# Performance work log

Hardware: AMD Instinct MI355X
Metric: run time of the kernel (lower is better)

The kernel has to match this reference:

```python
import jax, jax.numpy as jnp
import numpy as np
from jax import lax

H = 64      # hidden_size
VOC = 512   # num_embedding
L = 2       # num_layers


def layernorm(x, g, b, eps=1e-5):
    mu = jnp.mean(x, axis=-1, keepdims=True)
    var = jnp.mean((x - mu) ** 2, axis=-1, keepdims=True)
    return (x - mu) * lax.rsqrt(var + eps) * g + b


def conv3d(x, w, b):
    # x: [B, U, V, W, Cin] (channels-last), w: [3,3,3,Cin,Cout]
    return lax.conv_general_dilated(
        x, w, (1, 1, 1), 'SAME',
        dimension_numbers=('NDHWC', 'DHWIO', 'NDHWC')) + b


def setup_inputs() -> dict:
    key = jax.random.key(0)
    ks = jax.random.split(key, 8)
    f = lambda k, s, sc: jax.random.normal(k, s, jnp.float32) * sc
    return {
        'code': jax.random.randint(ks[0], (2, 5, 1, 8, 8, 8), 0, VOC),
        'ncode': jax.random.randint(ks[1], (2, 3, 1, 8, 8, 8), 0, VOC),
        'emb': f(ks[2], (VOC, H), 0.02),
        'win': f(ks[3], (L, 3, 3, 3, H, 4 * H), 0.05),
        'bin_': jnp.zeros((L, 4 * H), jnp.float32),
        'gin_w': jnp.ones((L, 4 * H), jnp.float32),
        'gin_b': jnp.zeros((L, 4 * H), jnp.float32),
        'wh': f(ks[4], (L, 3, 3, 3, H, 4 * H), 0.05),
        'bh': jnp.zeros((L, 4 * H), jnp.float32),
        'gh_w': jnp.ones((L, 4 * H), jnp.float32),
        'gh_b': jnp.zeros((L, 4 * H), jnp.float32),
        'w1': f(ks[5], (H, H), 0.05),
        'b1': jnp.zeros((H,), jnp.float32),
        'ln_g': jnp.ones((H,), jnp.float32),
        'ln_b': jnp.zeros((H,), jnp.float32),
        'w2': f(ks[6], (H, VOC), 0.05),
        'b2': jnp.zeros((VOC,), jnp.float32),
    }


def _forward(code, ncode, emb, win, bin_, gin_w, gin_b, wh, bh, gh_w, gh_b,
             w1, b1, ln_g, ln_b, w2, b2):
    N, Sn, C, U, V, W = ncode.shape
    x = jnp.concatenate([code, ncode[:, :-1]], axis=1)  # [N,S,C,U,V,W]
    S = x.shape[1]
    x = jnp.transpose(x, (0, 2, 1, 3, 4, 5)).reshape(N * C, S, U, V, W)
    h = emb[x]  # [NC, S, U, V, W, H]
    Hd = h.shape[-1]
    for i in range(L):
        # input-path conv is recurrence-free: batch it over all timesteps
        gi = layernorm(conv3d(h.reshape(N * C * S, U, V, W, Hd), win[i], bin_[i]),
                       gin_w[i], gin_b[i])
        gi = jnp.moveaxis(gi.reshape(N * C, S, U, V, W, 4 * Hd), 1, 0)  # [S,NC,U,V,W,4H]

        def step(carry, g, i=i):
            hx, cx = carry
            gates = g + layernorm(conv3d(hx, wh[i], bh[i]), gh_w[i], gh_b[i])
            ig, fg, cg, og = jnp.split(gates, 4, axis=-1)
            cx = jax.nn.sigmoid(fg) * cx + jax.nn.sigmoid(ig) * jnp.tanh(cg)
            hx = jax.nn.sigmoid(og) * jnp.tanh(cx)
            return (hx, cx), hx

        z = jnp.zeros((N * C, U, V, W, Hd), h.dtype)
        _, ys = lax.scan(step, (z, z), gi)
        h = jnp.moveaxis(ys, 0, 1)  # [NC,S,U,V,W,H]
    h = h[:, -Sn:].reshape(N, C, Sn, U, V, W, Hd)
    h = jnp.transpose(h, (0, 2, 1, 3, 4, 5, 6))  # [N,Sn,C,U,V,W,H]
    z = jax.nn.gelu(layernorm(h @ w1 + b1, ln_g, ln_b), approximate=False)
    logits = z @ w2 + b2  # [N,Sn,C,U,V,W,VOC]
    score = jnp.transpose(logits, (0, 6, 1, 2, 3, 4, 5))  # [N,VOC,Sn,C,U,V,W]
    logp = jax.nn.log_softmax(logits, axis=-1)
    loss = -jnp.mean(jnp.take_along_axis(logp, ncode[..., None], axis=-1))
    pred = jnp.argmax(score, axis=1)
    return score, loss, pred


def reference(code, ncode, emb, win, bin_, gin_w, gin_b, wh, bh, gh_w, gh_b,
              w1, b1, ln_g, ln_b, w2, b2):
    return _forward(code, ncode, emb, win, bin_, gin_w, gin_b, wh, bh,
                    gh_w, gh_b, w1, b1, ln_g, ln_b, w2, b2)
```

## Files before the change

### kernel.cpp

```cpp
#include <hip/hip_runtime.h>


typedef _Float16 f16;
typedef _Float16 f16x8 __attribute__((ext_vector_type(8)));
typedef float    f32x4 __attribute__((ext_vector_type(4)));

#define WSTRIDE 442368
#define WPT     884736
#define XSP     65536
#define HSP     458752
#define GPART   262144

__device__ __forceinline__ float wred_sum(float v) {
    #pragma unroll
    for (int o = 32; o > 0; o >>= 1) v += __shfl_down(v, o, 64);
    return __shfl(v, 0, 64);
}
__device__ __forceinline__ float fsig(float x)  { return 1.f / (1.f + __expf(-x)); }
__device__ __forceinline__ float ftanh(float x) { return 1.f - 2.f / (__expf(2.f*x) + 1.f); }

__global__ __launch_bounds__(256) void embed_kernel(
    const int* __restrict__ code, const int* __restrict__ ncode,
    const float* __restrict__ emb, f16* __restrict__ h)
{
    int e = blockIdx.x * 256 + threadIdx.x;
    int ch = e & 63;
    int pos = e >> 6;
    int vox = pos & 511;
    int t = pos >> 9;
    int s = t % 7, nc = t / 7;
    int tok = (s < 5) ? code[(nc*5 + s)*512 + vox]
                      : ncode[(nc*3 + (s-5))*512 + vox];
    float x = emb[tok*64 + ch];
    f16 hi = (f16)x;
    h[(size_t)pos*128 + ch]      = hi;
    h[(size_t)pos*128 + 64 + ch] = (f16)(x - (float)hi);
}

__global__ __launch_bounds__(256) void wsplit_kernel(
    const float* __restrict__ win, const float* __restrict__ wh,
    f16* __restrict__ wp)
{
    int b = blockIdx.x;
    int tensor = b / 27, tap = b % 27;
    const float* src = ((tensor & 1) ? wh : win) + (tensor >> 1) * WSTRIDE
                     + tap * 16384;
    int co = threadIdx.x;
    int sw = co & 7;
    #pragma unroll
    for (int hs = 0; hs < 2; ++hs) {
        f16* dst = wp + (((size_t)tensor*27 + tap)*2 + hs)*16384 + co*64;
        #pragma unroll
        for (int j = 0; j < 4; ++j) {
            f16x8 hi8, lo8;
            #pragma unroll
            for (int m = 0; m < 8; ++m) {
                float w = src[(hs*32 + j*8 + m)*256 + co] * 64.f;
                f16 hv = (f16)w;
                hi8[m] = hv;
                lo8[m] = (f16)(w - (float)hv);
            }
            *(f16x8*)(dst + ((j     ^ sw))*8) = hi8;
            *(f16x8*)(dst + (((4+j) ^ sw))*8) = lo8;
        }
    }
}

struct MJob { const f16* x; const f16* w; float* y; };
struct MJobs { MJob j[4]; };

__global__ __launch_bounds__(256, 2) void conv_mfma_kernel(MJobs js)
{
    const MJob J = js.j[blockIdx.y];
    __shared__ float4 smem[4096];
    f16* wbuf = (f16*)smem;

    const int bx = blockIdx.x;
    const int cog = bx & 3, u = (bx >> 2) & 7, slab = (bx >> 5) & 1, kb = bx >> 6;
    const int t = threadIdx.x, wid = t >> 6, l = t & 63;
    const int lv = (l >> 3) & 1, lw = l & 7, khi = l >> 4;

    const int gid = kb*4 + wid;
    const int g0  = (gid < 6) ? gid*7 : 42 + (gid - 6)*6;
    const int cnt = (gid < 6) ? 7 : 6;

    const f16* xbase = J.x + (size_t)slab * HSP;
    const f16* wjob  = J.w + (size_t)cog * 4096;
    f16* wmine = wbuf + wid * 8192;

    f16x8 wreg[8];
    auto wload = [&](int k) {
        const f16* src = wjob + (size_t)k * 16384 + l * 8;
        #pragma unroll
        for (int i = 0; i < 8; ++i) wreg[i] = *(const f16x8*)(src + i * 512);
    };
    auto wstore = [&](int b) {
        f16* dst = wmine + b * 4096 + l * 8;
        #pragma unroll
        for (int i = 0; i < 8; ++i) *(f16x8*)(dst + i * 512) = wreg[i];
    };

    wload(g0); wstore(0);

    f32x4 acc[4][4] = {};
    int cur = 0;
    for (int q = 0; q < cnt; ++q) {
        const int k = g0 + q;
        if (q + 1 < cnt) wload(k + 1);
        const int tap = k >> 1, hs = k & 1;
        const int du = tap / 9, rr = tap % 9, dv = rr / 3, dw = rr % 3;
        const int uu = u + du - 1;
        const bool uok = (unsigned)uu < 8u;
        const f16* xrow[4]; bool ok[4];
        #pragma unroll
        for (int a = 0; a < 4; ++a) {
            int vs = a*2 + lv + dv - 1, ws = lw + dw - 1;
            ok[a] = uok && (unsigned)vs < 8u && (unsigned)ws < 8u;
            xrow[a] = xbase + ((size_t)(uu*64 + vs*8 + ws) << 7) + khi*8;
        }
        const f16* wrow = wmine + cur*4096 + (l & 15)*64;
        const int schi = ((khi    ) ^ lw) * 8;
        const int sclo = ((4 + khi) ^ lw) * 8;
        f16x8 ahi[4], alo[4], bhi[4], blo[4];
        #pragma unroll
        for (int a = 0; a < 4; ++a) {
            f16x8 v = {0,0,0,0,0,0,0,0}, v2 = v;
            if (ok[a]) {
                v  = *(const f16x8*)(xrow[a] + hs*32);
                v2 = *(const f16x8*)(xrow[a] + 64 + hs*32);
            }
            ahi[a] = v; alo[a] = v2;
        }
        #pragma unroll
        for (int n = 0; n < 4; ++n) {
            bhi[n] = *(const f16x8*)(wrow + n*1024 + schi);
            blo[n] = *(const f16x8*)(wrow + n*1024 + sclo);
        }
        #pragma unroll
        for (int a = 0; a < 4; ++a)
            #pragma unroll
            for (int n = 0; n < 4; ++n)
                acc[a][n] = __builtin_amdgcn_mfma_f32_16x16x32_f16(
                    ahi[a], bhi[n], acc[a][n], 0, 0, 0);
        #pragma unroll
        for (int a = 0; a < 4; ++a)
            #pragma unroll
            for (int n = 0; n < 4; ++n)
                acc[a][n] = __builtin_amdgcn_mfma_f32_16x16x32_f16(
                    alo[a], bhi[n], acc[a][n], 0, 0, 0);
        #pragma unroll
        for (int a = 0; a < 4; ++a)
            #pragma unroll
            for (int n = 0; n < 4; ++n)
                acc[a][n] = __builtin_amdgcn_mfma_f32_16x16x32_f16(
                    ahi[a], blo[n], acc[a][n], 0, 0, 0);
        if (q + 1 < cnt) { wstore(cur ^ 1); cur ^= 1; }
    }

    f32x4* red = (f32x4*)smem;
    {
        f32x4* mine = red + (size_t)(wid * 64 + l) * 16;
        #pragma unroll
        for (int a = 0; a < 4; ++a)
            #pragma unroll
            for (int n = 0; n < 4; ++n)
                mine[(a * 4 + n) ^ (l & 15)] = acc[a][n];
    }
    __syncthreads();
    {
        float* yp = J.y + (size_t)kb * GPART;
        const int a = t >> 6, ll = t & 63;
        #pragma unroll
        for (int n = 0; n < 4; ++n) {
            const int ch = (a * 4 + n) ^ (ll & 15);
            f32x4 sv = red[(0 * 64 + ll) * 16 + ch]
                     + red[(1 * 64 + ll) * 16 + ch]
                     + red[(2 * 64 + ll) * 16 + ch]
                     + red[(3 * 64 + ll) * 16 + ch];
            const int co = cog * 64 + n * 16 + (ll & 15);
            #pragma unroll
            for (int r = 0; r < 4; ++r) {
                int vox = a * 16 + (ll >> 4) * 4 + r;
                yp[(size_t)(slab * 512 + u * 64 + vox) * 256 + co]
                    = sv[r] * 0.015625f;
            }
        }
    }
}

struct GJob {
    const float* giA; const float* giB;
    const float* ghA; const float* ghB;
    const float* bin; const float* bhb;
    const float* ginw; const float* ginb;
    const float* ghw;  const float* ghb;
    float* cx; f16* h16; int k; int k0;
};
__global__ __launch_bounds__(256) void gates_step_kernel(GJob ja, GJob jb)
{
    const GJob J = (blockIdx.y == 0) ? ja : jb;
    const int wid = threadIdx.x >> 6, lane = threadIdx.x & 63;
    const int row = blockIdx.x * 4 + wid;
    const int nc = row >> 9, vox = row & 511;

    const float* gA = J.giA + (size_t)row*256;
    const float* gB = J.giB + (size_t)row*256;
    float a0 = gA[lane]     + gB[lane]     + J.bin[lane];
    float a1 = gA[64+lane]  + gB[64+lane]  + J.bin[64+lane];
    float a2 = gA[128+lane] + gB[128+lane] + J.bin[128+lane];
    float a3 = gA[192+lane] + gB[192+lane] + J.bin[192+lane];
    float mu1 = wred_sum(a0+a1+a2+a3) * (1.f/256.f);
    float d0=a0-mu1, d1=a1-mu1, d2=a2-mu1, d3=a3-mu1;
    float v1 = wred_sum(d0*d0+d1*d1+d2*d2+d3*d3) * (1.f/256.f);
    float rs1 = rsqrtf(v1 + 1e-5f);

    float b0, b1, b2, b3;
    if (J.k0) {
        b0 = J.bhb[lane]; b1 = J.bhb[64+lane];
        b2 = J.bhb[128+lane]; b3 = J.bhb[192+lane];
    } else {
        const float* hA = J.ghA + (size_t)row*256;
        const float* hB = J.ghB + (size_t)row*256;
        b0 = hA[lane]     + hB[lane]     + J.bhb[lane];
        b1 = hA[64+lane]  + hB[64+lane]  + J.bhb[64+lane];
        b2 = hA[128+lane] + hB[128+lane] + J.bhb[128+lane];
        b3 = hA[192+lane] + hB[192+lane] + J.bhb[192+lane];
    }
    float mu2 = wred_sum(b0+b1+b2+b3) * (1.f/256.f);
    float e0=b0-mu2, e1=b1-mu2, e2=b2-mu2, e3=b3-mu2;
    float v2 = wred_sum(e0*e0+e1*e1+e2*e2+e3*e3) * (1.f/256.f);
    float rs2 = rsqrtf(v2 + 1e-5f);

    float Ig = d0*rs1*J.ginw[lane]     + J.ginb[lane]     + e0*rs2*J.ghw[lane]     + J.ghb[lane];
    float Fg = d1*rs1*J.ginw[64+lane]  + J.ginb[64+lane]  + e1*rs2*J.ghw[64+lane]  + J.ghb[64+lane];
    float Cg = d2*rs1*J.ginw[128+lane] + J.ginb[128+lane] + e2*rs2*J.ghw[128+lane] + J.ghb[128+lane];
    float Og = d3*rs1*J.ginw[192+lane] + J.ginb[192+lane] + e3*rs2*J.ghw[192+lane] + J.ghb[192+lane];

    float c_old = J.k0 ? 0.f : J.cx[(size_t)row*64 + lane];
    float c_new = fsig(Fg)*c_old + fsig(Ig)*ftanh(Cg);
    float h_new = fsig(Og)*ftanh(c_new);
    J.cx[(size_t)row*64 + lane] = c_new;
    size_t hb = ((size_t)(nc*7 + J.k)*512 + vox)*128 + lane;
    f16 hi = (f16)h_new;
    J.h16[hb]      = hi;
    J.h16[hb + 64] = (f16)(h_new - (float)hi);
}

__global__ __launch_bounds__(256) void head_kernel(
    const f16* __restrict__ h,
    const float* __restrict__ w1, const float* __restrict__ b1,
    const float* __restrict__ lng, const float* __restrict__ lnb,
    const float* __restrict__ w2, const float* __restrict__ b2,
    const int* __restrict__ ncode,
    float* __restrict__ out)
{
    __shared__ float hsm[16][64];
    __shared__ float zv[16][64];
    __shared__ float lg[10240];
    const int blk = blockIdx.x;
    const int n = blk / 96;
    const int sn = (blk / 32) % 3;
    const int vox0 = (blk & 31) * 16;
    const int t = threadIdx.x, wid = t >> 6, lane = t & 63;

    for (int idx = t; idx < 1024; idx += 256) {
        int vr = idx >> 6, ch = idx & 63;
        const f16* hv = h + (size_t)((n*7 + sn + 4)*512 + vox0 + vr)*128;
        hsm[vr][ch] = (float)hv[ch] + (float)hv[64 + ch];
    }
    __syncthreads();

    float yva[4], yvb[4];
    #pragma unroll
    for (int r = 0; r < 4; ++r) { yva[r] = b1[lane]; yvb[r] = 0.f; }
    for (int kk = 0; kk < 64; kk += 2) {
        float w1a = w1[kk*64 + lane], w1b = w1[(kk+1)*64 + lane];
        #pragma unroll
        for (int r = 0; r < 4; ++r) {
            yva[r] = fmaf(hsm[wid*4 + r][kk],     w1a, yva[r]);
            yvb[r] = fmaf(hsm[wid*4 + r][kk + 1], w1b, yvb[r]);
        }
    }
    #pragma unroll
    for (int r = 0; r < 4; ++r) {
        float yv = yva[r] + yvb[r];
        float mu = wred_sum(yv) * (1.f/64.f);
        float d = yv - mu;
        float var = wred_sum(d*d) * (1.f/64.f);
        float ln = d * rsqrtf(var + 1e-5f) * lng[lane] + lnb[lane];
        zv[wid*4 + r][lane] = 0.5f * ln * (1.f + erff(ln * 0.70710678118654752f));
    }
    __syncthreads();

    float l[4][8];
    #pragma unroll
    for (int r = 0; r < 4; ++r)
        #pragma unroll
        for (int j = 0; j < 8; ++j) l[r][j] = b2[j*64 + lane];
    for (int kk = 0; kk < 64; ++kk) {
        float wv[8];
        #pragma unroll
        for (int j = 0; j < 8; ++j) wv[j] = w2[kk*512 + j*64 + lane];
        #pragma unroll
        for (int r = 0; r < 4; ++r) {
            float zz = zv[wid*4 + r][kk];
            #pragma unroll
            for (int j = 0; j < 8; ++j) l[r][j] = fmaf(zz, wv[j], l[r][j]);
        }
    }
    #pragma unroll
    for (int r = 0; r < 4; ++r)
        #pragma unroll
        for (int j = 0; j < 8; ++j)
            lg[(j*64 + lane)*20 + wid*4 + r] = l[r][j];

    #pragma unroll
    for (int r = 0; r < 4; ++r) {
        float m = l[r][0]; int mi = lane;
        #pragma unroll
        for (int j = 1; j < 8; ++j)
            if (l[r][j] > m) { m = l[r][j]; mi = j*64 + lane; }
        #pragma unroll
        for (int o = 32; o > 0; o >>= 1) {
            float om = __shfl_down(m, o, 64);
            int   oi = __shfl_down(mi, o, 64);
            if (om > m || (om == m && oi < mi)) { m = om; mi = oi; }
        }
        float maxv = __shfl(m, 0, 64);
        int   maxi = __shfl(mi, 0, 64);
        float es = 0.f;
        #pragma unroll
        for (int j = 0; j < 8; ++j) es += __expf(l[r][j] - maxv);
        float sum = wred_sum(es);
        if (lane == 0) {
            int vox = vox0 + wid*4 + r;
            int target = ncode[(n*3 + sn)*512 + vox];
            float logp = lg[target*20 + wid*4 + r] - maxv - __logf(sum);
            atomicAdd(out + 1572864, -logp * (1.f/3072.f));
            out[1572865 + (n*3 + sn)*512 + vox] = (float)maxi;
        }
    }

    __syncthreads();
    for (int e = t; e < 2048; e += 256) {
        int co = e >> 2, p = e & 3;
        int base = co*20 + p*4;
        float4 o4 = { lg[base], lg[base+1], lg[base+2], lg[base+3] };
        *(float4*)(out + (size_t)((n*512 + co)*3 + sn)*512 + vox0 + p*4) = o4;
    }
}

extern "C" void kernel_launch(void* const* d_in, const int* in_sizes, int n_in,
                              void* d_out, int out_size, void* d_ws, size_t ws_size,
                              hipStream_t stream) {
    (void)in_sizes; (void)n_in; (void)out_size; (void)ws_size;
    const int*   code  = (const int*)d_in[0];
    const int*   ncode = (const int*)d_in[1];
    const float* emb   = (const float*)d_in[2];
    const float* win   = (const float*)d_in[3];
    const float* bin_  = (const float*)d_in[4];
    const float* gin_w = (const float*)d_in[5];
    const float* gin_b = (const float*)d_in[6];
    const float* wh    = (const float*)d_in[7];
    const float* bh    = (const float*)d_in[8];
    const float* gh_w  = (const float*)d_in[9];
    const float* gh_b  = (const float*)d_in[10];
    const float* w1    = (const float*)d_in[11];
    const float* b1    = (const float*)d_in[12];
    const float* ln_g  = (const float*)d_in[13];
    const float* ln_b  = (const float*)d_in[14];
    const float* w2    = (const float*)d_in[15];
    const float* b2    = (const float*)d_in[16];
    float* out = (float*)d_out;

    float* base  = (float*)d_ws;
    f16*   wp    = (f16*)base;
    f16*   h1    = (f16*)(base + 1769472);
    f16*   h2    = h1 + 917504;
    float* gi1   = base + 2686976;
    float* gi2   = gi1 + 2*GPART;
    float* ghat1 = gi2 + 2*GPART;
    float* ghat2 = ghat1 + 2*GPART;
    float* cx1   = ghat2 + 2*GPART;
    float* cx2   = cx1 + 65536;

    const f16* win0 = wp;
    const f16* wh0  = wp + WPT;
    const f16* win1 = wp + 2*WPT;
    const f16* wh1  = wp + 3*WPT;

    hipMemsetAsync(out + 1572864, 0, sizeof(float), stream);
    embed_kernel<<<1792, 256, 0, stream>>>(code, ncode, emb, h1);
    wsplit_kernel<<<108, 256, 0, stream>>>(win, wh, wp);

    {
        MJobs js{};
        js.j[0] = { h1, win0, gi1 };
        conv_mfma_kernel<<<dim3(128, 1), 256, 0, stream>>>(js);
    }

    for (int s = 0; s <= 7; ++s) {
        GJob g1 = { gi1, gi1 + GPART, ghat1, ghat1 + GPART, bin_, bh,
                    gin_w, gin_b, gh_w, gh_b, cx1, h1, s, s == 0 };
        GJob g2 = { gi2, gi2 + GPART, ghat2, ghat2 + GPART, bin_ + 256, bh + 256,
                    gin_w + 256, gin_b + 256, gh_w + 256, gh_b + 256,
                    cx2, h2, s - 1, s == 1 };
        if (s == 0)
            gates_step_kernel<<<dim3(256, 1), 256, 0, stream>>>(g1, g1);
        else if (s <= 6)
            gates_step_kernel<<<dim3(256, 2), 256, 0, stream>>>(g1, g2);
        else
            gates_step_kernel<<<dim3(256, 1), 256, 0, stream>>>(g2, g2);

        MJobs js{}; int nj = 0;
        if (s <= 5) js.j[nj++] = { h1 + (size_t)(s+1)*XSP, win0, gi1 };
        if (s <= 5) js.j[nj++] = { h1 + (size_t)s*XSP,     wh0,  ghat1 };
        if (s <= 6) js.j[nj++] = { h1 + (size_t)s*XSP,     win1, gi2 };
        if (s >= 1 && s <= 6)
                    js.j[nj++] = { h2 + (size_t)(s-1)*XSP, wh1,  ghat2 };
        if (nj > 0)
            conv_mfma_kernel<<<dim3(128, nj), 256, 0, stream>>>(js);
    }

    head_kernel<<<192, 256, 0, stream>>>(h2, w1, b1, ln_g, ln_b, w2, b2, ncode, out);
}
```

Before: 336.0 us.

## Split conv blocks over voxel halves, merge prep kernels, block-reduce loss atomics

```diff
diff --git a/kernel.cpp b/kernel.cpp
--- a/kernel.cpp
+++ b/kernel.cpp
@@ -19,49 +19,48 @@
 __device__ __forceinline__ float fsig(float x)  { return 1.f / (1.f + __expf(-x)); }
 __device__ __forceinline__ float ftanh(float x) { return 1.f - 2.f / (__expf(2.f*x) + 1.f); }
 
-__global__ __launch_bounds__(256) void embed_kernel(
+__global__ __launch_bounds__(256) void prep_kernel(
     const int* __restrict__ code, const int* __restrict__ ncode,
-    const float* __restrict__ emb, f16* __restrict__ h)
-{
-    int e = blockIdx.x * 256 + threadIdx.x;
-    int ch = e & 63;
-    int pos = e >> 6;
-    int vox = pos & 511;
-    int t = pos >> 9;
-    int s = t % 7, nc = t / 7;
-    int tok = (s < 5) ? code[(nc*5 + s)*512 + vox]
-                      : ncode[(nc*3 + (s-5))*512 + vox];
-    float x = emb[tok*64 + ch];
-    f16 hi = (f16)x;
-    h[(size_t)pos*128 + ch]      = hi;
-    h[(size_t)pos*128 + 64 + ch] = (f16)(x - (float)hi);
-}
-
-__global__ __launch_bounds__(256) void wsplit_kernel(
+    const float* __restrict__ emb, f16* __restrict__ h,
     const float* __restrict__ win, const float* __restrict__ wh,
     f16* __restrict__ wp)
 {
-    int b = blockIdx.x;
-    int tensor = b / 27, tap = b % 27;
-    const float* src = ((tensor & 1) ? wh : win) + (tensor >> 1) * WSTRIDE
-                     + tap * 16384;
-    int co = threadIdx.x;
-    int sw = co & 7;
-    #pragma unroll
-    for (int hs = 0; hs < 2; ++hs) {
-        f16* dst = wp + (((size_t)tensor*27 + tap)*2 + hs)*16384 + co*64;
-        #pragma unroll
-        for (int j = 0; j < 4; ++j) {
-            f16x8 hi8, lo8;
-            #pragma unroll
-            for (int m = 0; m < 8; ++m) {
-                float w = src[(hs*32 + j*8 + m)*256 + co] * 64.f;
-                f16 hv = (f16)w;
-                hi8[m] = hv;
-                lo8[m] = (f16)(w - (float)hv);
+    if (blockIdx.x < 1792) {
+        int e = blockIdx.x * 256 + threadIdx.x;
+        int ch = e & 63;
+        int pos = e >> 6;
+        int vox = pos & 511;
+        int t = pos >> 9;
+        int s = t % 7, nc = t / 7;
+        int tok = (s < 5) ? code[(nc*5 + s)*512 + vox]
+                          : ncode[(nc*3 + (s-5))*512 + vox];
+        float x = emb[tok*64 + ch];
+        f16 hi = (f16)x;
+        h[(size_t)pos*128 + ch]      = hi;
+        h[(size_t)pos*128 + 64 + ch] = (f16)(x - (float)hi);
+    } else {
+        int b = blockIdx.x - 1792;
+        int tensor = b / 27, tap = b % 27;
+        const float* src = ((tensor & 1) ? wh : win) + (tensor >> 1) * WSTRIDE
+                         + tap * 16384;
+        int co = threadIdx.x;
+        int sw = co & 7;
+        #pragma unroll
+        for (int hs = 0; hs < 2; ++hs) {
+            f16* dst = wp + (((size_t)tensor*27 + tap)*2 + hs)*16384 + co*64;
+            #pragma unroll
+            for (int j = 0; j < 4; ++j) {
+                f16x8 hi8, lo8;
+                #pragma unroll
+                for (int m = 0; m < 8; ++m) {
+                    float w = src[(hs*32 + j*8 + m)*256 + co] * 64.f;
+                    f16 hv = (f16)w;
+                    hi8[m] = hv;
+                    lo8[m] = (f16)(w - (float)hv);
+                }
+                *(f16x8*)(dst + ((j     ^ sw))*8) = hi8;
+                *(f16x8*)(dst + (((4+j) ^ sw))*8) = lo8;
             }
-            *(f16x8*)(dst + ((j     ^ sw))*8) = hi8;
-            *(f16x8*)(dst + (((4+j) ^ sw))*8) = lo8;
         }
     }
 }
@@ -69,14 +68,15 @@
 struct MJob { const f16* x; const f16* w; float* y; };
 struct MJobs { MJob j[4]; };
 
-__global__ __launch_bounds__(256, 2) void conv_mfma_kernel(MJobs js)
+__global__ __launch_bounds__(256, 3) void conv_mfma_kernel(MJobs js)
 {
     const MJob J = js.j[blockIdx.y];
-    __shared__ float4 smem[4096];
+    __shared__ float4 smem[2048];
     f16* wbuf = (f16*)smem;
 
     const int bx = blockIdx.x;
-    const int cog = bx & 3, u = (bx >> 2) & 7, slab = (bx >> 5) & 1, kb = bx >> 6;
+    const int cog = bx & 3, u = (bx >> 2) & 7, slab = (bx >> 5) & 1;
+    const int ah = (bx >> 6) & 1, kb = bx >> 7;
     const int t = threadIdx.x, wid = t >> 6, l = t & 63;
     const int lv = (l >> 3) & 1, lw = l & 7, khi = l >> 4;
 
@@ -86,7 +86,7 @@
 
     const f16* xbase = J.x + (size_t)slab * HSP;
     const f16* wjob  = J.w + (size_t)cog * 4096;
-    f16* wmine = wbuf + wid * 8192;
+    f16* wmine = wbuf + wid * 4096;
 
     f16x8 wreg[8];
     auto wload = [&](int k) {
@@ -94,16 +94,15 @@
         #pragma unroll
         for (int i = 0; i < 8; ++i) wreg[i] = *(const f16x8*)(src + i * 512);
     };
-    auto wstore = [&](int b) {
-        f16* dst = wmine + b * 4096 + l * 8;
+    auto wstore = [&]() {
+        f16* dst = wmine + l * 8;
         #pragma unroll
         for (int i = 0; i < 8; ++i) *(f16x8*)(dst + i * 512) = wreg[i];
     };
 
-    wload(g0); wstore(0);
-
-    f32x4 acc[4][4] = {};
-    int cur = 0;
+    wload(g0); wstore();
+
+    f32x4 acc[2][4] = {};
     for (int q = 0; q < cnt; ++q) {
         const int k = g0 + q;
         if (q + 1 < cnt) wload(k + 1);
@@ -111,25 +110,25 @@
         const int du = tap / 9, rr = tap % 9, dv = rr / 3, dw = rr % 3;
         const int uu = u + du - 1;
         const bool uok = (unsigned)uu < 8u;
-        const f16* xrow[4]; bool ok[4];
-        #pragma unroll
-        for (int a = 0; a < 4; ++a) {
-            int vs = a*2 + lv + dv - 1, ws = lw + dw - 1;
-            ok[a] = uok && (unsigned)vs < 8u && (unsigned)ws < 8u;
-            xrow[a] = xbase + ((size_t)(uu*64 + vs*8 + ws) << 7) + khi*8;
-        }
-        const f16* wrow = wmine + cur*4096 + (l & 15)*64;
+        const f16* xrow[2]; bool ok[2];
+        #pragma unroll
+        for (int aa = 0; aa < 2; ++aa) {
+            int vs = (ah*2 + aa)*2 + lv + dv - 1, ws = lw + dw - 1;
+            ok[aa] = uok && (unsigned)vs < 8u && (unsigned)ws < 8u;
+            xrow[aa] = xbase + ((size_t)(uu*64 + vs*8 + ws) << 7) + khi*8;
+        }
+        const f16* wrow = wmine + (l & 15)*64;
         const int schi = ((khi    ) ^ lw) * 8;
         const int sclo = ((4 + khi) ^ lw) * 8;
-        f16x8 ahi[4], alo[4], bhi[4], blo[4];
-        #pragma unroll
-        for (int a = 0; a < 4; ++a) {
+        f16x8 ahi[2], alo[2], bhi[4], blo[4];
+        #pragma unroll
+        for (int aa = 0; aa < 2; ++aa) {
             f16x8 v = {0,0,0,0,0,0,0,0}, v2 = v;
-            if (ok[a]) {
-                v  = *(const f16x8*)(xrow[a] + hs*32);
-                v2 = *(const f16x8*)(xrow[a] + 64 + hs*32);
+            if (ok[aa]) {
+                v  = *(const f16x8*)(xrow[aa] + hs*32);
+                v2 = *(const f16x8*)(xrow[aa] + 64 + hs*32);
             }
-            ahi[a] = v; alo[a] = v2;
+            ahi[aa] = v; alo[aa] = v2;
         }
         #pragma unroll
         for (int n = 0; n < 4; ++n) {
@@ -137,50 +136,51 @@
             blo[n] = *(const f16x8*)(wrow + n*1024 + sclo);
         }
         #pragma unroll
-        for (int a = 0; a < 4; ++a)
+        for (int aa = 0; aa < 2; ++aa)
             #pragma unroll
             for (int n = 0; n < 4; ++n)
-                acc[a][n] = __builtin_amdgcn_mfma_f32_16x16x32_f16(
-                    ahi[a], bhi[n], acc[a][n], 0, 0, 0);
-        #pragma unroll
-        for (int a = 0; a < 4; ++a)
+                acc[aa][n] = __builtin_amdgcn_mfma_f32_16x16x32_f16(
+                    ahi[aa], bhi[n], acc[aa][n], 0, 0, 0);
+        #pragma unroll
+        for (int aa = 0; aa < 2; ++aa)
             #pragma unroll
             for (int n = 0; n < 4; ++n)
-                acc[a][n] = __builtin_amdgcn_mfma_f32_16x16x32_f16(
-                    alo[a], bhi[n], acc[a][n], 0, 0, 0);
-        #pragma unroll
-        for (int a = 0; a < 4; ++a)
+                acc[aa][n] = __builtin_amdgcn_mfma_f32_16x16x32_f16(
+                    alo[aa], bhi[n], acc[aa][n], 0, 0, 0);
+        #pragma unroll
+        for (int aa = 0; aa < 2; ++aa)
             #pragma unroll
             for (int n = 0; n < 4; ++n)
-                acc[a][n] = __builtin_amdgcn_mfma_f32_16x16x32_f16(
-                    ahi[a], blo[n], acc[a][n], 0, 0, 0);
-        if (q + 1 < cnt) { wstore(cur ^ 1); cur ^= 1; }
+                acc[aa][n] = __builtin_amdgcn_mfma_f32_16x16x32_f16(
+                    ahi[aa], blo[n], acc[aa][n], 0, 0, 0);
+        if (q + 1 < cnt) wstore();
     }
 
     f32x4* red = (f32x4*)smem;
     {
-        f32x4* mine = red + (size_t)(wid * 64 + l) * 16;
-        #pragma unroll
-        for (int a = 0; a < 4; ++a)
+        f32x4* mine = red + (size_t)(wid * 64 + l) * 8;
+        #pragma unroll
+        for (int aa = 0; aa < 2; ++aa)
             #pragma unroll
             for (int n = 0; n < 4; ++n)
-                mine[(a * 4 + n) ^ (l & 15)] = acc[a][n];
+                mine[(aa * 4 + n) ^ lw] = acc[aa][n];
     }
     __syncthreads();
     {
         float* yp = J.y + (size_t)kb * GPART;
-        const int a = t >> 6, ll = t & 63;
-        #pragma unroll
-        for (int n = 0; n < 4; ++n) {
-            const int ch = (a * 4 + n) ^ (ll & 15);
-            f32x4 sv = red[(0 * 64 + ll) * 16 + ch]
-                     + red[(1 * 64 + ll) * 16 + ch]
-                     + red[(2 * 64 + ll) * 16 + ch]
-                     + red[(3 * 64 + ll) * 16 + ch];
+        const int aa = (t >> 7) & 1, nsel = (t >> 6) & 1, ll = t & 63;
+        #pragma unroll
+        for (int ni = 0; ni < 2; ++ni) {
+            const int n = nsel*2 + ni;
+            const int ch = (aa * 4 + n) ^ (ll & 7);
+            f32x4 sv = red[(0 * 64 + ll) * 8 + ch]
+                     + red[(1 * 64 + ll) * 8 + ch]
+                     + red[(2 * 64 + ll) * 8 + ch]
+                     + red[(3 * 64 + ll) * 8 + ch];
             const int co = cog * 64 + n * 16 + (ll & 15);
             #pragma unroll
             for (int r = 0; r < 4; ++r) {
-                int vox = a * 16 + (ll >> 4) * 4 + r;
+                int vox = (ah*2 + aa) * 16 + (ll >> 4) * 4 + r;
                 yp[(size_t)(slab * 512 + u * 64 + vox) * 256 + co]
                     = sv[r] * 0.015625f;
             }
@@ -257,6 +257,7 @@
     __shared__ float hsm[16][64];
     __shared__ float zv[16][64];
     __shared__ float lg[10240];
+    __shared__ float lsum[16];
     const int blk = blockIdx.x;
     const int n = blk / 96;
     const int sn = (blk / 32) % 3;
@@ -336,12 +337,18 @@
             int vox = vox0 + wid*4 + r;
             int target = ncode[(n*3 + sn)*512 + vox];
             float logp = lg[target*20 + wid*4 + r] - maxv - __logf(sum);
-            atomicAdd(out + 1572864, -logp * (1.f/3072.f));
+            lsum[wid*4 + r] = -logp * (1.f/3072.f);
             out[1572865 + (n*3 + sn)*512 + vox] = (float)maxi;
         }
     }
 
     __syncthreads();
+    if (t == 0) {
+        float s = 0.f;
+        #pragma unroll
+        for (int i = 0; i < 16; ++i) s += lsum[i];
+        atomicAdd(out + 1572864, s);
+    }
     for (int e = t; e < 2048; e += 256) {
         int co = e >> 2, p = e & 3;
         int base = co*20 + p*4;
@@ -390,13 +397,12 @@
     const f16* wh1  = wp + 3*WPT;
 
     hipMemsetAsync(out + 1572864, 0, sizeof(float), stream);
-    embed_kernel<<<1792, 256, 0, stream>>>(code, ncode, emb, h1);
-    wsplit_kernel<<<108, 256, 0, stream>>>(win, wh, wp);
+    prep_kernel<<<1900, 256, 0, stream>>>(code, ncode, emb, h1, win, wh, wp);
 
     {
         MJobs js{};
         js.j[0] = { h1, win0, gi1 };
-        conv_mfma_kernel<<<dim3(128, 1), 256, 0, stream>>>(js);
+        conv_mfma_kernel<<<dim3(256, 1), 256, 0, stream>>>(js);
     }
 
     for (int s = 0; s <= 7; ++s) {
@@ -419,7 +425,7 @@
         if (s >= 1 && s <= 6)
                     js.j[nj++] = { h2 + (size_t)(s-1)*XSP, wh1,  ghat2 };
         if (nj > 0)
-            conv_mfma_kernel<<<dim3(128, nj), 256, 0, stream>>>(js);
+            conv_mfma_kernel<<<dim3(256, nj), 256, 0, stream>>>(js);
     }
 
     head_kernel<<<192, 256, 0, stream>>>(h2, w1, b1, ln_g, ln_b, w2, b2, ncode, out);
```

After: 305.0 us. 9.2% less time.
